# Kernel tuning notes

Hardware: AMD Instinct MI355X
Metric: run time of the kernel (lower is better)

Reference implementation:

```python
import jax, jax.numpy as jnp
import numpy as np

BETA = 0.25
N_E = 4096
E_DIM = 64
B, T = 16, 1024


def setup_inputs() -> dict:
    key = jax.random.key(0)
    k1, k2 = jax.random.split(key)
    z = jax.random.normal(k1, (B, T, E_DIM), dtype=jnp.float32)
    # embedding.weight.data.uniform_(-1/n_e, 1/n_e)
    codebook = jax.random.uniform(k2, (N_E, E_DIM), dtype=jnp.float32,
                                  minval=-1.0 / N_E, maxval=1.0 / N_E)
    return {"z": z, "codebook": codebook}


def reference(z, codebook):
    # z: (B, T, e_dim), codebook: (n_e, e_dim)
    n_e, e_dim = codebook.shape
    zf = z.reshape(-1, e_dim)  # (N, e_dim)

    # d[n, k] = ||z_n||^2 + ||e_k||^2 - 2 z_n . e_k   -> (N, n_e)
    d = (jnp.sum(zf * zf, axis=1, keepdims=True)
         + jnp.sum(codebook * codebook, axis=1)
         - 2.0 * jnp.matmul(zf, codebook.T))

    idx = jnp.argmin(d, axis=1)                  # (N,) int
    z_q = codebook[idx].reshape(z.shape)         # (B, T, e_dim)

    sg = jax.lax.stop_gradient
    loss = jnp.mean((z_q - sg(z)) ** 2) + BETA * jnp.mean((sg(z_q) - z) ** 2)

    # straight-through estimator
    z_q_st = z + sg(z_q - z)

    # e_mean = mean over tokens of one-hot encodings == normalized code counts
    n_tokens = idx.shape[0]
    counts = jnp.zeros((n_e,), dtype=z.dtype).at[idx].add(1.0)
    e_mean = counts / n_tokens
    perplexity = jnp.exp(-jnp.sum(e_mean * jnp.log(e_mean + 1e-10)))

    return (loss, z_q_st, idx, perplexity)
```

## Files before the change

kernel.cpp:

```cpp
#include <hip/hip_runtime.h>
#include <math.h>

#define N_TOK   16384
#define EDIM    64
#define NE      4096
#define NSLICE  16
#define CSLICE  (NE / NSLICE)
#define CHUNK   128
#define TPB     256
#define TOKPT   2
#define ZQ_OFF  1
#define IDX_OFF (1 + N_TOK * EDIM)
#define PERP_OFF (IDX_OFF + N_TOK)

typedef unsigned long long u64;

__global__ __launch_bounds__(256) void norms_zero_kernel(
    const float* __restrict__ z, const float* __restrict__ cb,
    float* __restrict__ nz, float* __restrict__ ne,
    int* __restrict__ hist, float* __restrict__ lossAcc) {
#pragma clang fp contract(off)
    int i = blockIdx.x * 256 + threadIdx.x;
    if (i < NE) hist[i] = 0;
    if (i == 0) lossAcc[0] = 0.0f;
    const float* row;
    float* dst;
    if (i < N_TOK)            { row = z  + (size_t)i * EDIM;           dst = nz + i; }
    else if (i < N_TOK + NE)  { row = cb + (size_t)(i - N_TOK) * EDIM; dst = ne + (i - N_TOK); }
    else return;

    float r[8];
#pragma unroll
    for (int j = 0; j < 8; ++j) { float v = row[j]; r[j] = v * v; }
#pragma unroll
    for (int b = 8; b < 64; b += 8) {
#pragma unroll
        for (int j = 0; j < 8; ++j) { float v = row[b + j]; r[j] = r[j] + v * v; }
    }
    dst[0] = ((r[0] + r[1]) + (r[2] + r[3])) + ((r[4] + r[5]) + (r[6] + r[7]));
}

__global__ __launch_bounds__(256, 2) void dist_argmin_kernel(
    const float* __restrict__ z, const float* __restrict__ cb,
    const float* __restrict__ nz, const float* __restrict__ ne,
    u64* __restrict__ part) {
    __shared__ float se[CHUNK * EDIM];
    __shared__ float sne[CHUNK];
    const int tid    = threadIdx.x;
    const int token0 = blockIdx.x * (TPB * TOKPT) + tid;
    const int token1 = token0 + TPB;
    const int slice  = blockIdx.y;

    float zr0[EDIM], zr1[EDIM];
    {
        const float4* zp0 = (const float4*)(z + (size_t)token0 * EDIM);
        const float4* zp1 = (const float4*)(z + (size_t)token1 * EDIM);
#pragma unroll
        for (int j = 0; j < 16; ++j) {
            float4 v = zp0[j];
            zr0[4 * j + 0] = v.x; zr0[4 * j + 1] = v.y;
            zr0[4 * j + 2] = v.z; zr0[4 * j + 3] = v.w;
            float4 w = zp1[j];
            zr1[4 * j + 0] = w.x; zr1[4 * j + 1] = w.y;
            zr1[4 * j + 2] = w.z; zr1[4 * j + 3] = w.w;
        }
    }
    const float tnz0 = nz[token0];
    const float tnz1 = nz[token1];
    u64 best0 = ~0ull, best1 = ~0ull;

#pragma unroll 1
    for (int c = 0; c < CSLICE / CHUNK; ++c) {
        const int kbase = slice * CSLICE + c * CHUNK;
        {
            const float4* src = (const float4*)(cb + (size_t)kbase * EDIM);
            float4* dst = (float4*)se;
#pragma unroll
            for (int r = 0; r < (CHUNK * EDIM / 4) / TPB; ++r)
                dst[r * TPB + tid] = src[r * TPB + tid];
            if (tid < CHUNK / 4)
                ((float4*)sne)[tid] = ((const float4*)(ne + kbase))[tid];
        }
        __syncthreads();

#pragma unroll 1
        for (int k = 0; k < CHUNK; k += 2) {
            const float4* e0 = (const float4*)(se + (size_t)(k + 0) * EDIM);
            const float4* e1 = (const float4*)(se + (size_t)(k + 1) * EDIM);
            float d00 = 0.f, d01 = 0.f, d10 = 0.f, d11 = 0.f;
#pragma unroll
            for (int q = 0; q < 16; ++q) {
                float4 a = e0[q];
                float4 b = e1[q];
                d00 = __builtin_fmaf(zr0[4 * q + 0], a.x, d00);
                d00 = __builtin_fmaf(zr0[4 * q + 1], a.y, d00);
                d00 = __builtin_fmaf(zr0[4 * q + 2], a.z, d00);
                d00 = __builtin_fmaf(zr0[4 * q + 3], a.w, d00);
                d01 = __builtin_fmaf(zr0[4 * q + 0], b.x, d01);
                d01 = __builtin_fmaf(zr0[4 * q + 1], b.y, d01);
                d01 = __builtin_fmaf(zr0[4 * q + 2], b.z, d01);
                d01 = __builtin_fmaf(zr0[4 * q + 3], b.w, d01);
                d10 = __builtin_fmaf(zr1[4 * q + 0], a.x, d10);
                d10 = __builtin_fmaf(zr1[4 * q + 1], a.y, d10);
                d10 = __builtin_fmaf(zr1[4 * q + 2], a.z, d10);
                d10 = __builtin_fmaf(zr1[4 * q + 3], a.w, d10);
                d11 = __builtin_fmaf(zr1[4 * q + 0], b.x, d11);
                d11 = __builtin_fmaf(zr1[4 * q + 1], b.y, d11);
                d11 = __builtin_fmaf(zr1[4 * q + 2], b.z, d11);
                d11 = __builtin_fmaf(zr1[4 * q + 3], b.w, d11);
            }
            const float s0 = sne[k + 0], s1 = sne[k + 1];
            float t00 = __builtin_fmaf(-2.0f, d00, tnz0 + s0);
            float t01 = __builtin_fmaf(-2.0f, d01, tnz0 + s1);
            float t10 = __builtin_fmaf(-2.0f, d10, tnz1 + s0);
            float t11 = __builtin_fmaf(-2.0f, d11, tnz1 + s1);
            u64 p;
            p = ((u64)__float_as_uint(t00) << 32) | (u64)(kbase + k + 0); if (p < best0) best0 = p;
            p = ((u64)__float_as_uint(t01) << 32) | (u64)(kbase + k + 1); if (p < best0) best0 = p;
            p = ((u64)__float_as_uint(t10) << 32) | (u64)(kbase + k + 0); if (p < best1) best1 = p;
            p = ((u64)__float_as_uint(t11) << 32) | (u64)(kbase + k + 1); if (p < best1) best1 = p;
        }
        __syncthreads();
    }
    part[(size_t)slice * N_TOK + token0] = best0;
    part[(size_t)slice * N_TOK + token1] = best1;
}

__global__ __launch_bounds__(256) void reduce_gather_kernel(
    const float* __restrict__ z, const float* __restrict__ cb,
    const u64* __restrict__ part, int* __restrict__ hist,
    float* __restrict__ lossAcc, float* __restrict__ out) {
    const int t = blockIdx.x * 256 + threadIdx.x;
    u64 best = part[t];
#pragma unroll
    for (int s = 1; s < NSLICE; ++s) {
        u64 p = part[(size_t)s * N_TOK + t];
        if (p < best) best = p;
    }
    const int idx = (int)(best & 0xFFFFFFFFull);
    out[IDX_OFF + t] = (float)idx;
    atomicAdd(&hist[idx], 1);

    const float4* ev = (const float4*)(cb + (size_t)idx * EDIM);
    const float4* zv = (const float4*)(z + (size_t)t * EDIM);
    float* o = out + ZQ_OFF + (size_t)t * EDIM;
    float acc = 0.0f;
#pragma unroll
    for (int j = 0; j < 16; ++j) {
        float4 e = ev[j], zz = zv[j];
        float d;
        d = e.x - zz.x; o[4 * j + 0] = zz.x + d; acc = __builtin_fmaf(d, d, acc);
        d = e.y - zz.y; o[4 * j + 1] = zz.y + d; acc = __builtin_fmaf(d, d, acc);
        d = e.z - zz.z; o[4 * j + 2] = zz.z + d; acc = __builtin_fmaf(d, d, acc);
        d = e.w - zz.w; o[4 * j + 3] = zz.w + d; acc = __builtin_fmaf(d, d, acc);
    }
    __shared__ float red[256];
    red[threadIdx.x] = acc;
    __syncthreads();
    for (int s = 128; s > 0; s >>= 1) {
        if (threadIdx.x < s) red[threadIdx.x] += red[threadIdx.x + s];
        __syncthreads();
    }
    if (threadIdx.x == 0) atomicAdd(lossAcc, red[0]);
}

__global__ __launch_bounds__(256) void finalize_kernel(
    const int* __restrict__ hist, const float* __restrict__ lossAcc,
    float* __restrict__ out) {
    __shared__ float red[256];
    float acc = 0.0f;
    for (int i = threadIdx.x; i < NE; i += 256) {
        float e = (float)hist[i] * (1.0f / 16384.0f);
        acc += e * logf(e + 1e-10f);
    }
    red[threadIdx.x] = acc;
    __syncthreads();
    for (int s = 128; s > 0; s >>= 1) {
        if (threadIdx.x < s) red[threadIdx.x] += red[threadIdx.x + s];
        __syncthreads();
    }
    if (threadIdx.x == 0) {
        out[PERP_OFF] = expf(-red[0]);
        float m = lossAcc[0] * (1.0f / 1048576.0f);
        out[0] = m + 0.25f * m;
    }
}

extern "C" void kernel_launch(void* const* d_in, const int* in_sizes, int n_in,
                              void* d_out, int out_size, void* d_ws, size_t ws_size,
                              hipStream_t stream) {
    const float* z  = (const float*)d_in[0];
    const float* cb = (const float*)d_in[1];
    float* out = (float*)d_out;

    char* ws = (char*)d_ws;
    u64*   part    = (u64*)ws;
    float* nz      = (float*)(ws + (size_t)NSLICE * N_TOK * 8);
    float* ne      = nz + N_TOK;
    int*   hist    = (int*)(ne + NE);
    float* lossAcc = (float*)(hist + NE);

    hipLaunchKernelGGL(norms_zero_kernel, dim3(80), dim3(256), 0, stream,
                       z, cb, nz, ne, hist, lossAcc);
    hipLaunchKernelGGL(dist_argmin_kernel,
                       dim3(N_TOK / (TPB * TOKPT), NSLICE), dim3(TPB), 0, stream,
                       z, cb, nz, ne, part);
    hipLaunchKernelGGL(reduce_gather_kernel, dim3(64), dim3(256), 0, stream,
                       z, cb, part, hist, lossAcc, out);
    hipLaunchKernelGGL(finalize_kernel, dim3(1), dim3(256), 0, stream,
                       hist, lossAcc, out);
}
```

Baseline: 199.3 us.

## Fuse norm computation into distance kernel, use packed FMA, and raise slice count

Drops the separate norms/zeroing kernel. Token and codebook norms are now computed inside the distance/argmin kernel, and histogram/loss zeroing is done by slice-0 blocks. The inner dot product uses inline v_pk_fma_f32 so one instruction handles both tokens, aiming to halve VALU FMA issue. When the workspace allows, the codebook is split into 32 slices instead of 16 to raise grid parallelism. The cost is recomputing codebook norms in every block and a larger partial-result buffer for the reduce kernel to read.

After: 225.2 us. 13.0% more time.

```diff
diff --git a/kernel.cpp b/kernel.cpp
--- a/kernel.cpp
+++ b/kernel.cpp
@@ -4,8 +4,6 @@
 #define N_TOK   16384
 #define EDIM    64
 #define NE      4096
-#define NSLICE  16
-#define CSLICE  (NE / NSLICE)
 #define CHUNK   128
 #define TPB     256
 #define TOKPT   2
@@ -14,36 +12,13 @@
 #define PERP_OFF (IDX_OFF + N_TOK)
 
 typedef unsigned long long u64;
-
-__global__ __launch_bounds__(256) void norms_zero_kernel(
-    const float* __restrict__ z, const float* __restrict__ cb,
-    float* __restrict__ nz, float* __restrict__ ne,
-    int* __restrict__ hist, float* __restrict__ lossAcc) {
-#pragma clang fp contract(off)
-    int i = blockIdx.x * 256 + threadIdx.x;
-    if (i < NE) hist[i] = 0;
-    if (i == 0) lossAcc[0] = 0.0f;
-    const float* row;
-    float* dst;
-    if (i < N_TOK)            { row = z  + (size_t)i * EDIM;           dst = nz + i; }
-    else if (i < N_TOK + NE)  { row = cb + (size_t)(i - N_TOK) * EDIM; dst = ne + (i - N_TOK); }
-    else return;
-
-    float r[8];
-#pragma unroll
-    for (int j = 0; j < 8; ++j) { float v = row[j]; r[j] = v * v; }
-#pragma unroll
-    for (int b = 8; b < 64; b += 8) {
-#pragma unroll
-        for (int j = 0; j < 8; ++j) { float v = row[b + j]; r[j] = r[j] + v * v; }
-    }
-    dst[0] = ((r[0] + r[1]) + (r[2] + r[3])) + ((r[4] + r[5]) + (r[6] + r[7]));
-}
+typedef float v2f __attribute__((ext_vector_type(2)));
+typedef float v4f __attribute__((ext_vector_type(4)));
 
 __global__ __launch_bounds__(256, 2) void dist_argmin_kernel(
     const float* __restrict__ z, const float* __restrict__ cb,
-    const float* __restrict__ nz, const float* __restrict__ ne,
-    u64* __restrict__ part) {
+    u64* __restrict__ part, int* __restrict__ hist,
+    float* __restrict__ lossAcc, int csl) {
     __shared__ float se[CHUNK * EDIM];
     __shared__ float sne[CHUNK];
     const int tid    = threadIdx.x;
@@ -51,69 +26,114 @@
     const int token1 = token0 + TPB;
     const int slice  = blockIdx.y;
 
-    float zr0[EDIM], zr1[EDIM];
+    if (slice == 0) {
+        int gid = blockIdx.x * TPB + tid;
+        if (gid < NE) hist[gid] = 0;
+        if (gid == NE) lossAcc[0] = 0.0f;
+    }
+
+    v2f zp[EDIM];
     {
-        const float4* zp0 = (const float4*)(z + (size_t)token0 * EDIM);
-        const float4* zp1 = (const float4*)(z + (size_t)token1 * EDIM);
-#pragma unroll
-        for (int j = 0; j < 16; ++j) {
-            float4 v = zp0[j];
-            zr0[4 * j + 0] = v.x; zr0[4 * j + 1] = v.y;
-            zr0[4 * j + 2] = v.z; zr0[4 * j + 3] = v.w;
-            float4 w = zp1[j];
-            zr1[4 * j + 0] = w.x; zr1[4 * j + 1] = w.y;
-            zr1[4 * j + 2] = w.z; zr1[4 * j + 3] = w.w;
-        }
-    }
-    const float tnz0 = nz[token0];
-    const float tnz1 = nz[token1];
+        const v4f* zp0 = (const v4f*)(z + (size_t)token0 * EDIM);
+        const v4f* zp1 = (const v4f*)(z + (size_t)token1 * EDIM);
+#pragma unroll
+        for (int q = 0; q < 16; ++q) {
+            v4f a = zp0[q], b = zp1[q];
+            zp[4 * q + 0].x = a.x; zp[4 * q + 0].y = b.x;
+            zp[4 * q + 1].x = a.y; zp[4 * q + 1].y = b.y;
+            zp[4 * q + 2].x = a.z; zp[4 * q + 2].y = b.z;
+            zp[4 * q + 3].x = a.w; zp[4 * q + 3].y = b.w;
+        }
+    }
+    float tnz0, tnz1;
+    {
+#pragma clang fp contract(off)
+        float r0[8], r1[8];
+#pragma unroll
+        for (int j = 0; j < 8; ++j) {
+            float v0 = zp[j].x, v1 = zp[j].y;
+            r0[j] = v0 * v0; r1[j] = v1 * v1;
+        }
+#pragma unroll
+        for (int b = 8; b < 64; b += 8) {
+#pragma unroll
+            for (int j = 0; j < 8; ++j) {
+                float v0 = zp[b + j].x, v1 = zp[b + j].y;
+                r0[j] = r0[j] + v0 * v0; r1[j] = r1[j] + v1 * v1;
+            }
+        }
+        tnz0 = ((r0[0] + r0[1]) + (r0[2] + r0[3])) + ((r0[4] + r0[5]) + (r0[6] + r0[7]));
+        tnz1 = ((r1[0] + r1[1]) + (r1[2] + r1[3])) + ((r1[4] + r1[5]) + (r1[6] + r1[7]));
+    }
+
     u64 best0 = ~0ull, best1 = ~0ull;
-
+    const int kend = slice * csl + csl;
 #pragma unroll 1
-    for (int c = 0; c < CSLICE / CHUNK; ++c) {
-        const int kbase = slice * CSLICE + c * CHUNK;
+    for (int kbase = slice * csl; kbase < kend; kbase += CHUNK) {
         {
-            const float4* src = (const float4*)(cb + (size_t)kbase * EDIM);
-            float4* dst = (float4*)se;
+            const v4f* src = (const v4f*)(cb + (size_t)kbase * EDIM);
+            v4f* dst = (v4f*)se;
 #pragma unroll
             for (int r = 0; r < (CHUNK * EDIM / 4) / TPB; ++r)
                 dst[r * TPB + tid] = src[r * TPB + tid];
-            if (tid < CHUNK / 4)
-                ((float4*)sne)[tid] = ((const float4*)(ne + kbase))[tid];
+        }
+        if (tid < CHUNK) {
+#pragma clang fp contract(off)
+            const v4f* cr = (const v4f*)(cb + (size_t)(kbase + tid) * EDIM);
+            float r[8];
+            {
+                v4f c0 = cr[0], c1 = cr[1];
+                r[0] = c0.x * c0.x; r[1] = c0.y * c0.y;
+                r[2] = c0.z * c0.z; r[3] = c0.w * c0.w;
+                r[4] = c1.x * c1.x; r[5] = c1.y * c1.y;
+                r[6] = c1.z * c1.z; r[7] = c1.w * c1.w;
+            }
+#pragma unroll
+            for (int b = 1; b < 8; ++b) {
+                v4f a = cr[2 * b], d = cr[2 * b + 1];
+                r[0] = r[0] + a.x * a.x; r[1] = r[1] + a.y * a.y;
+                r[2] = r[2] + a.z * a.z; r[3] = r[3] + a.w * a.w;
+                r[4] = r[4] + d.x * d.x; r[5] = r[5] + d.y * d.y;
+                r[6] = r[6] + d.z * d.z; r[7] = r[7] + d.w * d.w;
+            }
+            sne[tid] = ((r[0] + r[1]) + (r[2] + r[3])) + ((r[4] + r[5]) + (r[6] + r[7]));
         }
         __syncthreads();
 
 #pragma unroll 1
         for (int k = 0; k < CHUNK; k += 2) {
-            const float4* e0 = (const float4*)(se + (size_t)(k + 0) * EDIM);
-            const float4* e1 = (const float4*)(se + (size_t)(k + 1) * EDIM);
-            float d00 = 0.f, d01 = 0.f, d10 = 0.f, d11 = 0.f;
+            const v4f* e0 = (const v4f*)(se + (size_t)(k + 0) * EDIM);
+            const v4f* e1 = (const v4f*)(se + (size_t)(k + 1) * EDIM);
+            v2f a0 = {0.f, 0.f}, a1 = {0.f, 0.f};
 #pragma unroll
             for (int q = 0; q < 16; ++q) {
-                float4 a = e0[q];
-                float4 b = e1[q];
-                d00 = __builtin_fmaf(zr0[4 * q + 0], a.x, d00);
-                d00 = __builtin_fmaf(zr0[4 * q + 1], a.y, d00);
-                d00 = __builtin_fmaf(zr0[4 * q + 2], a.z, d00);
-                d00 = __builtin_fmaf(zr0[4 * q + 3], a.w, d00);
-                d01 = __builtin_fmaf(zr0[4 * q + 0], b.x, d01);
-                d01 = __builtin_fmaf(zr0[4 * q + 1], b.y, d01);
-                d01 = __builtin_fmaf(zr0[4 * q + 2], b.z, d01);
-                d01 = __builtin_fmaf(zr0[4 * q + 3], b.w, d01);
-                d10 = __builtin_fmaf(zr1[4 * q + 0], a.x, d10);
-                d10 = __builtin_fmaf(zr1[4 * q + 1], a.y, d10);
-                d10 = __builtin_fmaf(zr1[4 * q + 2], a.z, d10);
-                d10 = __builtin_fmaf(zr1[4 * q + 3], a.w, d10);
-                d11 = __builtin_fmaf(zr1[4 * q + 0], b.x, d11);
-                d11 = __builtin_fmaf(zr1[4 * q + 1], b.y, d11);
-                d11 = __builtin_fmaf(zr1[4 * q + 2], b.z, d11);
-                d11 = __builtin_fmaf(zr1[4 * q + 3], b.w, d11);
+                v4f A = e0[q], B = e1[q];
+                v2f Alo = __builtin_shufflevector(A, A, 0, 1);
+                v2f Ahi = __builtin_shufflevector(A, A, 2, 3);
+                v2f Blo = __builtin_shufflevector(B, B, 0, 1);
+                v2f Bhi = __builtin_shufflevector(B, B, 2, 3);
+                asm("v_pk_fma_f32 %0, %1, %2, %0 op_sel:[0,0,0] op_sel_hi:[1,0,1]"
+                    : "+v"(a0) : "v"(zp[4 * q + 0]), "v"(Alo));
+                asm("v_pk_fma_f32 %0, %1, %2, %0 op_sel:[0,1,0] op_sel_hi:[1,1,1]"
+                    : "+v"(a0) : "v"(zp[4 * q + 1]), "v"(Alo));
+                asm("v_pk_fma_f32 %0, %1, %2, %0 op_sel:[0,0,0] op_sel_hi:[1,0,1]"
+                    : "+v"(a0) : "v"(zp[4 * q + 2]), "v"(Ahi));
+                asm("v_pk_fma_f32 %0, %1, %2, %0 op_sel:[0,1,0] op_sel_hi:[1,1,1]"
+                    : "+v"(a0) : "v"(zp[4 * q + 3]), "v"(Ahi));
+                asm("v_pk_fma_f32 %0, %1, %2, %0 op_sel:[0,0,0] op_sel_hi:[1,0,1]"
+                    : "+v"(a1) : "v"(zp[4 * q + 0]), "v"(Blo));
+                asm("v_pk_fma_f32 %0, %1, %2, %0 op_sel:[0,1,0] op_sel_hi:[1,1,1]"
+                    : "+v"(a1) : "v"(zp[4 * q + 1]), "v"(Blo));
+                asm("v_pk_fma_f32 %0, %1, %2, %0 op_sel:[0,0,0] op_sel_hi:[1,0,1]"
+                    : "+v"(a1) : "v"(zp[4 * q + 2]), "v"(Bhi));
+                asm("v_pk_fma_f32 %0, %1, %2, %0 op_sel:[0,1,0] op_sel_hi:[1,1,1]"
+                    : "+v"(a1) : "v"(zp[4 * q + 3]), "v"(Bhi));
             }
             const float s0 = sne[k + 0], s1 = sne[k + 1];
-            float t00 = __builtin_fmaf(-2.0f, d00, tnz0 + s0);
-            float t01 = __builtin_fmaf(-2.0f, d01, tnz0 + s1);
-            float t10 = __builtin_fmaf(-2.0f, d10, tnz1 + s0);
-            float t11 = __builtin_fmaf(-2.0f, d11, tnz1 + s1);
+            float t00 = __builtin_fmaf(-2.0f, a0.x, tnz0 + s0);
+            float t01 = __builtin_fmaf(-2.0f, a1.x, tnz0 + s1);
+            float t10 = __builtin_fmaf(-2.0f, a0.y, tnz1 + s0);
+            float t11 = __builtin_fmaf(-2.0f, a1.y, tnz1 + s1);
             u64 p;
             p = ((u64)__float_as_uint(t00) << 32) | (u64)(kbase + k + 0); if (p < best0) best0 = p;
             p = ((u64)__float_as_uint(t01) << 32) | (u64)(kbase + k + 1); if (p < best0) best0 = p;
@@ -129,11 +149,10 @@
 __global__ __launch_bounds__(256) void reduce_gather_kernel(
     const float* __restrict__ z, const float* __restrict__ cb,
     const u64* __restrict__ part, int* __restrict__ hist,
-    float* __restrict__ lossAcc, float* __restrict__ out) {
+    float* __restrict__ lossAcc, float* __restrict__ out, int nslice) {
     const int t = blockIdx.x * 256 + threadIdx.x;
     u64 best = part[t];
-#pragma unroll
-    for (int s = 1; s < NSLICE; ++s) {
+    for (int s = 1; s < nslice; ++s) {
         u64 p = part[(size_t)s * N_TOK + t];
         if (p < best) best = p;
     }
@@ -193,20 +212,20 @@
     const float* cb = (const float*)d_in[1];
     float* out = (float*)d_out;
 
+    const size_t need32 = (size_t)32 * N_TOK * 8 + (size_t)(NE + 1) * 4;
+    const int nslice = (ws_size >= need32) ? 32 : 16;
+    const int csl = NE / nslice;
+
     char* ws = (char*)d_ws;
     u64*   part    = (u64*)ws;
-    float* nz      = (float*)(ws + (size_t)NSLICE * N_TOK * 8);
-    float* ne      = nz + N_TOK;
-    int*   hist    = (int*)(ne + NE);
+    int*   hist    = (int*)(ws + (size_t)nslice * N_TOK * 8);
     float* lossAcc = (float*)(hist + NE);
 
-    hipLaunchKernelGGL(norms_zero_kernel, dim3(80), dim3(256), 0, stream,
-                       z, cb, nz, ne, hist, lossAcc);
     hipLaunchKernelGGL(dist_argmin_kernel,
-                       dim3(N_TOK / (TPB * TOKPT), NSLICE), dim3(TPB), 0, stream,
-                       z, cb, nz, ne, part);
+                       dim3(N_TOK / (TPB * TOKPT), nslice), dim3(TPB), 0, stream,
+                       z, cb, part, hist, lossAcc, csl);
     hipLaunchKernelGGL(reduce_gather_kernel, dim3(64), dim3(256), 0, stream,
-                       z, cb, part, hist, lossAcc, out);
+                       z, cb, part, hist, lossAcc, out, nslice);
     hipLaunchKernelGGL(finalize_kernel, dim3(1), dim3(256), 0, stream,
                        hist, lossAcc, out);
 }
```
